# Performance work log

Hardware: AMD Instinct MI355X
Metric: run time of the kernel (lower is better)

The kernel has to match this reference:

```python
import jax, jax.numpy as jnp
import numpy as np

B, LQ, LK, H, A = 32, 2048, 2048, 1024, 512


def setup_inputs() -> dict:
    key = jax.random.key(0)
    ks = jax.random.split(key, 5)
    s = 1.0 / np.sqrt(H)
    return {
        "query": jax.random.normal(ks[0], (B, LQ, H), jnp.float32),
        "key": jax.random.normal(ks[1], (B, LK, H), jnp.float32),
        "Wq": jax.random.normal(ks[2], (H, A), jnp.float32) * s,
        "bq": jnp.zeros((A,), jnp.float32),
        "Wk": jax.random.normal(ks[3], (H, A), jnp.float32) * s,
        "bk": jnp.zeros((A,), jnp.float32),
        "Wv": jax.random.normal(ks[4], (A, 1), jnp.float32) * (1.0 / np.sqrt(A)),
        "bv": jnp.zeros((1,), jnp.float32),
    }


def reference(query, key, Wq, bq, Wk, bk, Wv, bv):
    # Linear projections
    Qp = jnp.einsum("bqh,ha->bqa", query, Wq) + bq          # [B, LQ, A]
    Kp = jnp.einsum("bkh,ha->bka", key, Wk) + bk            # [B, LK, A]
    # Score matrix Q(query) @ K(key)^T
    alpha_mat = jnp.einsum("bqa,bka->bqk", Qp, Kp)          # [B, LQ, LK]
    # Sum over query dim, softmax over key dim
    alpha = jax.nn.softmax(alpha_mat.sum(axis=1, keepdims=True), axis=2)  # [B, 1, LK]
    # Per-key scalar head V applied to projected keys, then weighted combine
    v = jnp.einsum("bka,ao->bko", Kp, Wv) + bv              # [B, LK, 1]
    x = jnp.matmul(alpha, v)[:, 0, :]                        # [B, 1]
    return x
```

## Files before the change

kernel.cpp:

```cpp
#include <hip/hip_runtime.h>
#include <math.h>

#define NB 32
#define LQ 2048
#define LK 2048
#define HD 1024
#define AD 512
#define QCH 32

__global__ void __launch_bounds__(256)
k1_stream(const float* __restrict__ query, const float* __restrict__ Wk,
          const float* __restrict__ Wv, const float* __restrict__ bk,
          const float* __restrict__ bv, float* __restrict__ partial,
          float* __restrict__ wv_eff, float* __restrict__ c_v) {
    const int bid = blockIdx.x;
    const int t = threadIdx.x;
    if (bid < NB * QCH) {
        int b = bid / QCH, qc = bid % QCH;
        const int QPC = LQ / QCH;
        float4 a0 = {0.f,0.f,0.f,0.f}, a1 = {0.f,0.f,0.f,0.f};
        float4 a2 = {0.f,0.f,0.f,0.f}, a3 = {0.f,0.f,0.f,0.f};
        const float4* src = (const float4*)(query + ((size_t)b * LQ + (size_t)qc * QPC) * HD);
        for (int q = 0; q < QPC; q += 4) {
            float4 v0 = src[(size_t)(q + 0) * (HD / 4) + t];
            float4 v1 = src[(size_t)(q + 1) * (HD / 4) + t];
            float4 v2 = src[(size_t)(q + 2) * (HD / 4) + t];
            float4 v3 = src[(size_t)(q + 3) * (HD / 4) + t];
            a0.x += v0.x; a0.y += v0.y; a0.z += v0.z; a0.w += v0.w;
            a1.x += v1.x; a1.y += v1.y; a1.z += v1.z; a1.w += v1.w;
            a2.x += v2.x; a2.y += v2.y; a2.z += v2.z; a2.w += v2.w;
            a3.x += v3.x; a3.y += v3.y; a3.z += v3.z; a3.w += v3.w;
        }
        float4 acc = {(a0.x + a1.x) + (a2.x + a3.x), (a0.y + a1.y) + (a2.y + a3.y),
                      (a0.z + a1.z) + (a2.z + a3.z), (a0.w + a1.w) + (a2.w + a3.w)};
        ((float4*)(partial + ((size_t)qc * NB + b) * HD))[t] = acc;
    } else if (bid < NB * QCH + 16) {
        int w = t >> 6, lane = t & 63;
        int gw = (bid - NB * QCH) * 4 + w;
        const float4* vv = (const float4*)Wv;
        for (int r = 0; r < 16; ++r) {
            int h = gw * 16 + r;
            const float4* wr = (const float4*)(Wk + (size_t)h * AD);
            double acc = 0.0;
            #pragma unroll
            for (int j = 0; j < 2; ++j) {
                int f = lane + 64 * j;
                float4 w4 = wr[f];
                float4 v4 = vv[f];
                acc += (double)w4.x * v4.x + (double)w4.y * v4.y
                     + (double)w4.z * v4.z + (double)w4.w * v4.w;
            }
            #pragma unroll
            for (int off = 32; off > 0; off >>= 1) acc += __shfl_down(acc, off);
            if (lane == 0) wv_eff[h] = (float)acc;
        }
    } else if (t < 64) {
        int lane = t;
        const float4* br = (const float4*)bk;
        const float4* vv = (const float4*)Wv;
        double acc = 0.0;
        #pragma unroll
        for (int j = 0; j < 2; ++j) {
            int f = lane + 64 * j;
            float4 b4 = br[f];
            float4 v4 = vv[f];
            acc += (double)b4.x * v4.x + (double)b4.y * v4.y
                 + (double)b4.z * v4.z + (double)b4.w * v4.w;
        }
        #pragma unroll
        for (int off = 32; off > 0; off >>= 1) acc += __shfl_down(acc, off);
        if (lane == 0) c_v[0] = (float)(acc + (double)bv[0]);
    }
}

__global__ void __launch_bounds__(256)
k2_qsum(const float* __restrict__ partial, const float* __restrict__ Wq,
        const float* __restrict__ bq, float* __restrict__ qsum) {
    __shared__ float sq[HD];
    __shared__ double red[4][64];
    int b = blockIdx.x >> 3;
    int a0 = (blockIdx.x & 7) * 64;
    int t = threadIdx.x;

    #pragma unroll
    for (int c = 0; c < 4; ++c) {
        int h = t + c * 256;
        float acc = 0.f;
        #pragma unroll 4
        for (int qc = 0; qc < QCH; ++qc)
            acc += partial[((size_t)qc * NB + b) * HD + h];
        sq[h] = acc;
    }
    __syncthreads();

    int w = t >> 6, lane = t & 63;
    int a = a0 + lane;
    const float* wp = Wq + a;
    double c0 = 0.0, c1 = 0.0, c2 = 0.0, c3 = 0.0;
    int hbase = w * 256;
    for (int i = 0; i < 256; i += 4) {
        int h = hbase + i;
        c0 += (double)sq[h]     * wp[(size_t)h * AD];
        c1 += (double)sq[h + 1] * wp[(size_t)(h + 1) * AD];
        c2 += (double)sq[h + 2] * wp[(size_t)(h + 2) * AD];
        c3 += (double)sq[h + 3] * wp[(size_t)(h + 3) * AD];
    }
    red[w][lane] = ((c0 + c1) + (c2 + c3));
    __syncthreads();
    if (t < 64) {
        double s = red[0][t] + red[1][t] + red[2][t] + red[3][t];
        qsum[(size_t)b * AD + a0 + t] = (float)(s + (double)LQ * bq[a0 + t]);
    }
}

__global__ void __launch_bounds__(256)
k3_weff(const float* __restrict__ qsum, const float* __restrict__ Wk,
        float* __restrict__ wk_eff) {
    int w = threadIdx.x >> 6, lane = threadIdx.x & 63;
    int widx = blockIdx.x * 4 + w;
    int base = widx * 4;
    for (int r = 0; r < 4; r += 2) {
        int idx0 = base + r;
        int b = idx0 >> 10, h0 = idx0 & (HD - 1);
        const float4* r0 = (const float4*)(Wk + (size_t)h0 * AD);
        const float4* r1 = (const float4*)(Wk + (size_t)(h0 + 1) * AD);
        const float4* qs = (const float4*)(qsum + (size_t)b * AD);
        double a0 = 0.0, a1 = 0.0;
        #pragma unroll
        for (int j = 0; j < 2; ++j) {
            int f = lane + 64 * j;
            float4 w0 = r0[f];
            float4 w1 = r1[f];
            float4 q4 = qs[f];
            a0 += (double)w0.x * q4.x + (double)w0.y * q4.y
                + (double)w0.z * q4.z + (double)w0.w * q4.w;
            a1 += (double)w1.x * q4.x + (double)w1.y * q4.y
                + (double)w1.z * q4.z + (double)w1.w * q4.w;
        }
        #pragma unroll
        for (int off = 32; off > 0; off >>= 1) {
            a0 += __shfl_down(a0, off);
            a1 += __shfl_down(a1, off);
        }
        if (lane == 0) {
            wk_eff[idx0]     = (float)a0;
            wk_eff[idx0 + 1] = (float)a1;
        }
    }
}

__global__ void __launch_bounds__(256)
k4_scores(const float* __restrict__ key, const float* __restrict__ wk_eff,
          const float* __restrict__ wv_eff, const float* __restrict__ c_v,
          float* __restrict__ scores, float* __restrict__ vvals) {
    __shared__ float lwk[HD];
    __shared__ float lwv[HD];
    const int bid = blockIdx.x;
    const int b = bid >> 6;
    const int k0 = (bid & 63) * 32;
    const int t = threadIdx.x;
    for (int i = t; i < HD; i += 256) {
        lwk[i] = wk_eff[(size_t)b * HD + i];
        lwv[i] = wv_eff[i];
    }
    __syncthreads();
    int w = t >> 6, lane = t & 63;
    double cv = (double)c_v[0];
    const float4* lwk4 = (const float4*)lwk;
    const float4* lwv4 = (const float4*)lwv;
    for (int rp = 0; rp < 2; ++rp) {
        int k = k0 + w * 8 + rp * 4;
        const float4* kr0 = (const float4*)(key + ((size_t)b * LK + k) * HD);
        const float4* kr1 = kr0 + (HD / 4);
        const float4* kr2 = kr0 + 2 * (HD / 4);
        const float4* kr3 = kr0 + 3 * (HD / 4);
        double sc0 = 0.0, vv0 = 0.0, sc1 = 0.0, vv1 = 0.0;
        double sc2 = 0.0, vv2 = 0.0, sc3 = 0.0, vv3 = 0.0;
        #pragma unroll
        for (int j = 0; j < 4; ++j) {
            int f = lane + 64 * j;
            float4 k0v = kr0[f];
            float4 k1v = kr1[f];
            float4 k2v = kr2[f];
            float4 k3v = kr3[f];
            float4 wk4 = lwk4[f];
            float4 wv4 = lwv4[f];
            sc0 += (double)k0v.x * wk4.x + (double)k0v.y * wk4.y
                 + (double)k0v.z * wk4.z + (double)k0v.w * wk4.w;
            vv0 += (double)k0v.x * wv4.x + (double)k0v.y * wv4.y
                 + (double)k0v.z * wv4.z + (double)k0v.w * wv4.w;
            sc1 += (double)k1v.x * wk4.x + (double)k1v.y * wk4.y
                 + (double)k1v.z * wk4.z + (double)k1v.w * wk4.w;
            vv1 += (double)k1v.x * wv4.x + (double)k1v.y * wv4.y
                 + (double)k1v.z * wv4.z + (double)k1v.w * wv4.w;
            sc2 += (double)k2v.x * wk4.x + (double)k2v.y * wk4.y
                 + (double)k2v.z * wk4.z + (double)k2v.w * wk4.w;
            vv2 += (double)k2v.x * wv4.x + (double)k2v.y * wv4.y
                 + (double)k2v.z * wv4.z + (double)k2v.w * wv4.w;
            sc3 += (double)k3v.x * wk4.x + (double)k3v.y * wk4.y
                 + (double)k3v.z * wk4.z + (double)k3v.w * wk4.w;
            vv3 += (double)k3v.x * wv4.x + (double)k3v.y * wv4.y
                 + (double)k3v.z * wv4.z + (double)k3v.w * wv4.w;
        }
        #pragma unroll
        for (int off = 32; off > 0; off >>= 1) {
            sc0 += __shfl_down(sc0, off);
            vv0 += __shfl_down(vv0, off);
            sc1 += __shfl_down(sc1, off);
            vv1 += __shfl_down(vv1, off);
            sc2 += __shfl_down(sc2, off);
            vv2 += __shfl_down(vv2, off);
            sc3 += __shfl_down(sc3, off);
            vv3 += __shfl_down(vv3, off);
        }
        if (lane == 0) {
            size_t base = (size_t)b * LK + k;
            scores[base]     = (float)sc0;  vvals[base]     = (float)(vv0 + cv);
            scores[base + 1] = (float)sc1;  vvals[base + 1] = (float)(vv1 + cv);
            scores[base + 2] = (float)sc2;  vvals[base + 2] = (float)(vv2 + cv);
            scores[base + 3] = (float)sc3;  vvals[base + 3] = (float)(vv3 + cv);
        }
    }
}

__global__ void __launch_bounds__(256)
k5_softmax(const float* __restrict__ scores, const float* __restrict__ vvals,
           float* __restrict__ out) {
    int b = blockIdx.x;
    int t = threadIdx.x;
    __shared__ float smax_sh[4];
    __shared__ double num_sh[4], den_sh[4];
    const float* sr = scores + (size_t)b * LK;
    const float* vr = vvals  + (size_t)b * LK;
    float m = -INFINITY;
    for (int k = t; k < LK; k += 256) m = fmaxf(m, sr[k]);
    #pragma unroll
    for (int off = 32; off > 0; off >>= 1) m = fmaxf(m, __shfl_down(m, off));
    int w = t >> 6, lane = t & 63;
    if (lane == 0) smax_sh[w] = m;
    __syncthreads();
    float gm = fmaxf(fmaxf(smax_sh[0], smax_sh[1]), fmaxf(smax_sh[2], smax_sh[3]));
    double num = 0.0, den = 0.0;
    for (int k = t; k < LK; k += 256) {
        double e = exp((double)(sr[k] - gm));
        den += e;
        num += e * (double)vr[k];
    }
    #pragma unroll
    for (int off = 32; off > 0; off >>= 1) {
        num += __shfl_down(num, off);
        den += __shfl_down(den, off);
    }
    if (lane == 0) { num_sh[w] = num; den_sh[w] = den; }
    __syncthreads();
    if (t == 0) {
        double N = num_sh[0] + num_sh[1] + num_sh[2] + num_sh[3];
        double D = den_sh[0] + den_sh[1] + den_sh[2] + den_sh[3];
        out[b] = (float)(N / D);
    }
}

extern "C" void kernel_launch(void* const* d_in, const int* in_sizes, int n_in,
                              void* d_out, int out_size, void* d_ws, size_t ws_size,
                              hipStream_t stream) {
    const float* query = (const float*)d_in[0];
    const float* key   = (const float*)d_in[1];
    const float* Wq    = (const float*)d_in[2];
    const float* bq    = (const float*)d_in[3];
    const float* Wk    = (const float*)d_in[4];
    const float* bk    = (const float*)d_in[5];
    const float* Wv    = (const float*)d_in[6];
    const float* bv    = (const float*)d_in[7];
    float* out = (float*)d_out;

    float* ws = (float*)d_ws;
    size_t off = 0;
    float* partial = ws + off; off += (size_t)QCH * NB * HD;
    float* qsum    = ws + off; off += (size_t)NB * AD;
    float* wk_eff  = ws + off; off += (size_t)NB * HD;
    float* wv_eff  = ws + off; off += (size_t)HD;
    float* c_v     = ws + off; off += 1;
    float* scores  = ws + off; off += (size_t)NB * LK;
    float* vvals   = ws + off; off += (size_t)NB * LK;

    hipLaunchKernelGGL(k1_stream, dim3(NB * QCH + 16 + 1), dim3(256), 0, stream,
                       query, Wk, Wv, bk, bv, partial, wv_eff, c_v);
    hipLaunchKernelGGL(k2_qsum, dim3(256), dim3(256), 0, stream,
                       partial, Wq, bq, qsum);
    hipLaunchKernelGGL(k3_weff, dim3(2048), dim3(256), 0, stream,
                       qsum, Wk, wk_eff);
    hipLaunchKernelGGL(k4_scores, dim3(NB * (LK / 32)), dim3(256), 0, stream,
                       key, wk_eff, wv_eff, c_v, scores, vvals);
    hipLaunchKernelGGL(k5_softmax, dim3(NB), dim3(256), 0, stream,
                       scores, vvals, out);
}
```

Measured before the change: 147.9 us.

## Fuse five kernels into two using last-block-done atomic counters

Merges the query-sum reduction, the Wq projection and the Wk effective-weight computation into the streaming kernel, and the softmax into the scores kernel. Each uses a per-batch atomic counter so that the last block to finish does the follow-up work. The streaming kernel now runs 512-thread blocks with float2 loads, and the counters are cleared with a memset. This removes three kernel launches and the intermediate round trips, but the fused tails (about 4 MB of weight reads per batch) now run on only 32 blocks instead of hundreds, which can lengthen the critical path.

```diff
diff --git a/kernel.cpp b/kernel.cpp
--- a/kernel.cpp
+++ b/kernel.cpp
@@ -8,38 +8,107 @@
 #define AD 512
 #define QCH 32
 
-__global__ void __launch_bounds__(256)
-k1_stream(const float* __restrict__ query, const float* __restrict__ Wk,
+__global__ void __launch_bounds__(512)
+k1_stream(const float* __restrict__ query, const float* __restrict__ Wq,
+          const float* __restrict__ bq, const float* __restrict__ Wk,
           const float* __restrict__ Wv, const float* __restrict__ bk,
-          const float* __restrict__ bv, float* __restrict__ partial,
-          float* __restrict__ wv_eff, float* __restrict__ c_v) {
+          const float* __restrict__ bv,
+          float* __restrict__ partial, float* __restrict__ wk_eff,
+          float* __restrict__ wv_eff, float* __restrict__ c_v,
+          int* __restrict__ cnt) {
+    __shared__ float sq[HD];
+    __shared__ float qs[AD];
+    __shared__ int isLast;
     const int bid = blockIdx.x;
     const int t = threadIdx.x;
+
     if (bid < NB * QCH) {
         int b = bid / QCH, qc = bid % QCH;
         const int QPC = LQ / QCH;
-        float4 a0 = {0.f,0.f,0.f,0.f}, a1 = {0.f,0.f,0.f,0.f};
-        float4 a2 = {0.f,0.f,0.f,0.f}, a3 = {0.f,0.f,0.f,0.f};
-        const float4* src = (const float4*)(query + ((size_t)b * LQ + (size_t)qc * QPC) * HD);
+        float2 a0 = {0.f,0.f}, a1 = {0.f,0.f}, a2 = {0.f,0.f}, a3 = {0.f,0.f};
+        const float2* src = (const float2*)(query + ((size_t)b * LQ + (size_t)qc * QPC) * HD);
         for (int q = 0; q < QPC; q += 4) {
-            float4 v0 = src[(size_t)(q + 0) * (HD / 4) + t];
-            float4 v1 = src[(size_t)(q + 1) * (HD / 4) + t];
-            float4 v2 = src[(size_t)(q + 2) * (HD / 4) + t];
-            float4 v3 = src[(size_t)(q + 3) * (HD / 4) + t];
-            a0.x += v0.x; a0.y += v0.y; a0.z += v0.z; a0.w += v0.w;
-            a1.x += v1.x; a1.y += v1.y; a1.z += v1.z; a1.w += v1.w;
-            a2.x += v2.x; a2.y += v2.y; a2.z += v2.z; a2.w += v2.w;
-            a3.x += v3.x; a3.y += v3.y; a3.z += v3.z; a3.w += v3.w;
-        }
-        float4 acc = {(a0.x + a1.x) + (a2.x + a3.x), (a0.y + a1.y) + (a2.y + a3.y),
-                      (a0.z + a1.z) + (a2.z + a3.z), (a0.w + a1.w) + (a2.w + a3.w)};
-        ((float4*)(partial + ((size_t)qc * NB + b) * HD))[t] = acc;
+            float2 v0 = src[(size_t)(q + 0) * (HD / 2) + t];
+            float2 v1 = src[(size_t)(q + 1) * (HD / 2) + t];
+            float2 v2 = src[(size_t)(q + 2) * (HD / 2) + t];
+            float2 v3 = src[(size_t)(q + 3) * (HD / 2) + t];
+            a0.x += v0.x; a0.y += v0.y;
+            a1.x += v1.x; a1.y += v1.y;
+            a2.x += v2.x; a2.y += v2.y;
+            a3.x += v3.x; a3.y += v3.y;
+        }
+        float sx = (a0.x + a1.x) + (a2.x + a3.x);
+        float sy = (a0.y + a1.y) + (a2.y + a3.y);
+        float* dst = partial + ((size_t)qc * NB + b) * HD + 2 * t;
+        atomicExch(dst,     sx);
+        atomicExch(dst + 1, sy);
+        asm volatile("s_waitcnt vmcnt(0)" ::: "memory");
+        __syncthreads();
+        if (t == 0) {
+            int old = atomicAdd(&cnt[b], 1);
+            isLast = (old == QCH - 1) ? 1 : 0;
+        }
+        __syncthreads();
+        if (!isLast) return;
+
+        #pragma unroll
+        for (int c = 0; c < 2; ++c) {
+            int h = t + c * 512;
+            float a = 0.f;
+            #pragma unroll 4
+            for (int q2 = 0; q2 < QCH; ++q2)
+                a += atomicAdd(partial + ((size_t)q2 * NB + b) * HD + h, 0.0f);
+            sq[h] = a;
+        }
+        __syncthreads();
+        {
+            const float* wp = Wq + t;
+            double c0 = 0.0, c1 = 0.0, c2 = 0.0, c3 = 0.0;
+            for (int h = 0; h < HD; h += 4) {
+                c0 += (double)sq[h]     * wp[(size_t)h * AD];
+                c1 += (double)sq[h + 1] * wp[(size_t)(h + 1) * AD];
+                c2 += (double)sq[h + 2] * wp[(size_t)(h + 2) * AD];
+                c3 += (double)sq[h + 3] * wp[(size_t)(h + 3) * AD];
+            }
+            qs[t] = (float)(((c0 + c1) + (c2 + c3)) + (double)LQ * (double)bq[t]);
+        }
+        __syncthreads();
+        {
+            int w = t >> 6, lane = t & 63;
+            const float4* qs4 = (const float4*)qs;
+            for (int r = 0; r < 128; r += 2) {
+                int h0 = w * 128 + r;
+                const float4* r0 = (const float4*)(Wk + (size_t)h0 * AD);
+                const float4* r1 = (const float4*)(Wk + (size_t)(h0 + 1) * AD);
+                double d0 = 0.0, d1 = 0.0;
+                #pragma unroll
+                for (int j = 0; j < 2; ++j) {
+                    int f = lane + 64 * j;
+                    float4 w0 = r0[f];
+                    float4 w1 = r1[f];
+                    float4 q4 = qs4[f];
+                    d0 += (double)w0.x * q4.x + (double)w0.y * q4.y
+                        + (double)w0.z * q4.z + (double)w0.w * q4.w;
+                    d1 += (double)w1.x * q4.x + (double)w1.y * q4.y
+                        + (double)w1.z * q4.z + (double)w1.w * q4.w;
+                }
+                #pragma unroll
+                for (int off = 32; off > 0; off >>= 1) {
+                    d0 += __shfl_down(d0, off);
+                    d1 += __shfl_down(d1, off);
+                }
+                if (lane == 0) {
+                    wk_eff[(size_t)b * HD + h0]     = (float)d0;
+                    wk_eff[(size_t)b * HD + h0 + 1] = (float)d1;
+                }
+            }
+        }
     } else if (bid < NB * QCH + 16) {
         int w = t >> 6, lane = t & 63;
-        int gw = (bid - NB * QCH) * 4 + w;
+        int gw = (bid - NB * QCH) * 8 + w;
         const float4* vv = (const float4*)Wv;
-        for (int r = 0; r < 16; ++r) {
-            int h = gw * 16 + r;
+        for (int r = 0; r < 8; ++r) {
+            int h = gw * 8 + r;
             const float4* wr = (const float4*)(Wk + (size_t)h * AD);
             double acc = 0.0;
             #pragma unroll
@@ -74,87 +143,15 @@
 }
 
 __global__ void __launch_bounds__(256)
-k2_qsum(const float* __restrict__ partial, const float* __restrict__ Wq,
-        const float* __restrict__ bq, float* __restrict__ qsum) {
-    __shared__ float sq[HD];
-    __shared__ double red[4][64];
-    int b = blockIdx.x >> 3;
-    int a0 = (blockIdx.x & 7) * 64;
-    int t = threadIdx.x;
-
-    #pragma unroll
-    for (int c = 0; c < 4; ++c) {
-        int h = t + c * 256;
-        float acc = 0.f;
-        #pragma unroll 4
-        for (int qc = 0; qc < QCH; ++qc)
-            acc += partial[((size_t)qc * NB + b) * HD + h];
-        sq[h] = acc;
-    }
-    __syncthreads();
-
-    int w = t >> 6, lane = t & 63;
-    int a = a0 + lane;
-    const float* wp = Wq + a;
-    double c0 = 0.0, c1 = 0.0, c2 = 0.0, c3 = 0.0;
-    int hbase = w * 256;
-    for (int i = 0; i < 256; i += 4) {
-        int h = hbase + i;
-        c0 += (double)sq[h]     * wp[(size_t)h * AD];
-        c1 += (double)sq[h + 1] * wp[(size_t)(h + 1) * AD];
-        c2 += (double)sq[h + 2] * wp[(size_t)(h + 2) * AD];
-        c3 += (double)sq[h + 3] * wp[(size_t)(h + 3) * AD];
-    }
-    red[w][lane] = ((c0 + c1) + (c2 + c3));
-    __syncthreads();
-    if (t < 64) {
-        double s = red[0][t] + red[1][t] + red[2][t] + red[3][t];
-        qsum[(size_t)b * AD + a0 + t] = (float)(s + (double)LQ * bq[a0 + t]);
-    }
-}
-
-__global__ void __launch_bounds__(256)
-k3_weff(const float* __restrict__ qsum, const float* __restrict__ Wk,
-        float* __restrict__ wk_eff) {
-    int w = threadIdx.x >> 6, lane = threadIdx.x & 63;
-    int widx = blockIdx.x * 4 + w;
-    int base = widx * 4;
-    for (int r = 0; r < 4; r += 2) {
-        int idx0 = base + r;
-        int b = idx0 >> 10, h0 = idx0 & (HD - 1);
-        const float4* r0 = (const float4*)(Wk + (size_t)h0 * AD);
-        const float4* r1 = (const float4*)(Wk + (size_t)(h0 + 1) * AD);
-        const float4* qs = (const float4*)(qsum + (size_t)b * AD);
-        double a0 = 0.0, a1 = 0.0;
-        #pragma unroll
-        for (int j = 0; j < 2; ++j) {
-            int f = lane + 64 * j;
-            float4 w0 = r0[f];
-            float4 w1 = r1[f];
-            float4 q4 = qs[f];
-            a0 += (double)w0.x * q4.x + (double)w0.y * q4.y
-                + (double)w0.z * q4.z + (double)w0.w * q4.w;
-            a1 += (double)w1.x * q4.x + (double)w1.y * q4.y
-                + (double)w1.z * q4.z + (double)w1.w * q4.w;
-        }
-        #pragma unroll
-        for (int off = 32; off > 0; off >>= 1) {
-            a0 += __shfl_down(a0, off);
-            a1 += __shfl_down(a1, off);
-        }
-        if (lane == 0) {
-            wk_eff[idx0]     = (float)a0;
-            wk_eff[idx0 + 1] = (float)a1;
-        }
-    }
-}
-
-__global__ void __launch_bounds__(256)
-k4_scores(const float* __restrict__ key, const float* __restrict__ wk_eff,
+k2_scores(const float* __restrict__ key, const float* __restrict__ wk_eff,
           const float* __restrict__ wv_eff, const float* __restrict__ c_v,
-          float* __restrict__ scores, float* __restrict__ vvals) {
+          float* __restrict__ scores, float* __restrict__ vvals,
+          int* __restrict__ cnt2, float* __restrict__ out) {
     __shared__ float lwk[HD];
     __shared__ float lwv[HD];
+    __shared__ int isLast;
+    __shared__ float smax_sh[4];
+    __shared__ double num_sh[4], den_sh[4];
     const int bid = blockIdx.x;
     const int b = bid >> 6;
     const int k0 = (bid & 63) * 32;
@@ -215,36 +212,46 @@
         }
         if (lane == 0) {
             size_t base = (size_t)b * LK + k;
-            scores[base]     = (float)sc0;  vvals[base]     = (float)(vv0 + cv);
-            scores[base + 1] = (float)sc1;  vvals[base + 1] = (float)(vv1 + cv);
-            scores[base + 2] = (float)sc2;  vvals[base + 2] = (float)(vv2 + cv);
-            scores[base + 3] = (float)sc3;  vvals[base + 3] = (float)(vv3 + cv);
-        }
-    }
-}
-
-__global__ void __launch_bounds__(256)
-k5_softmax(const float* __restrict__ scores, const float* __restrict__ vvals,
-           float* __restrict__ out) {
-    int b = blockIdx.x;
-    int t = threadIdx.x;
-    __shared__ float smax_sh[4];
-    __shared__ double num_sh[4], den_sh[4];
-    const float* sr = scores + (size_t)b * LK;
-    const float* vr = vvals  + (size_t)b * LK;
-    float m = -INFINITY;
-    for (int k = t; k < LK; k += 256) m = fmaxf(m, sr[k]);
+            atomicExch(&scores[base],     (float)sc0);
+            atomicExch(&vvals [base],     (float)(vv0 + cv));
+            atomicExch(&scores[base + 1], (float)sc1);
+            atomicExch(&vvals [base + 1], (float)(vv1 + cv));
+            atomicExch(&scores[base + 2], (float)sc2);
+            atomicExch(&vvals [base + 2], (float)(vv2 + cv));
+            atomicExch(&scores[base + 3], (float)sc3);
+            atomicExch(&vvals [base + 3], (float)(vv3 + cv));
+        }
+    }
+    asm volatile("s_waitcnt vmcnt(0)" ::: "memory");
+    __syncthreads();
+    if (t == 0) {
+        int old = atomicAdd(&cnt2[b], 1);
+        isLast = (old == 63) ? 1 : 0;
+    }
+    __syncthreads();
+    if (!isLast) return;
+
+    float s8[8], v8[8];
+    #pragma unroll
+    for (int i = 0; i < 8; ++i) {
+        int k = t + i * 256;
+        s8[i] = atomicAdd(&scores[(size_t)b * LK + k], 0.0f);
+        v8[i] = atomicAdd(&vvals [(size_t)b * LK + k], 0.0f);
+    }
+    float m = s8[0];
+    #pragma unroll
+    for (int i = 1; i < 8; ++i) m = fmaxf(m, s8[i]);
     #pragma unroll
     for (int off = 32; off > 0; off >>= 1) m = fmaxf(m, __shfl_down(m, off));
-    int w = t >> 6, lane = t & 63;
     if (lane == 0) smax_sh[w] = m;
     __syncthreads();
     float gm = fmaxf(fmaxf(smax_sh[0], smax_sh[1]), fmaxf(smax_sh[2], smax_sh[3]));
     double num = 0.0, den = 0.0;
-    for (int k = t; k < LK; k += 256) {
-        double e = exp((double)(sr[k] - gm));
+    #pragma unroll
+    for (int i = 0; i < 8; ++i) {
+        double e = exp((double)s8[i] - (double)gm);
         den += e;
-        num += e * (double)vr[k];
+        num += e * (double)v8[i];
     }
     #pragma unroll
     for (int off = 32; off > 0; off >>= 1) {
@@ -276,21 +283,17 @@
     float* ws = (float*)d_ws;
     size_t off = 0;
     float* partial = ws + off; off += (size_t)QCH * NB * HD;
-    float* qsum    = ws + off; off += (size_t)NB * AD;
     float* wk_eff  = ws + off; off += (size_t)NB * HD;
     float* wv_eff  = ws + off; off += (size_t)HD;
     float* c_v     = ws + off; off += 1;
     float* scores  = ws + off; off += (size_t)NB * LK;
     float* vvals   = ws + off; off += (size_t)NB * LK;
-
-    hipLaunchKernelGGL(k1_stream, dim3(NB * QCH + 16 + 1), dim3(256), 0, stream,
-                       query, Wk, Wv, bk, bv, partial, wv_eff, c_v);
-    hipLaunchKernelGGL(k2_qsum, dim3(256), dim3(256), 0, stream,
-                       partial, Wq, bq, qsum);
-    hipLaunchKernelGGL(k3_weff, dim3(2048), dim3(256), 0, stream,
-                       qsum, Wk, wk_eff);
-    hipLaunchKernelGGL(k4_scores, dim3(NB * (LK / 32)), dim3(256), 0, stream,
-                       key, wk_eff, wv_eff, c_v, scores, vvals);
-    hipLaunchKernelGGL(k5_softmax, dim3(NB), dim3(256), 0, stream,
-                       scores, vvals, out);
+    int*   cnt     = (int*)(ws + off); off += 2 * NB;
+
+    hipMemsetAsync(cnt, 0, 2 * NB * sizeof(int), stream);
+    hipLaunchKernelGGL(k1_stream, dim3(NB * QCH + 16 + 1), dim3(512), 0, stream,
+                       query, Wq, bq, Wk, Wv, bk, bv,
+                       partial, wk_eff, wv_eff, c_v, cnt);
+    hipLaunchKernelGGL(k2_scores, dim3(NB * (LK / 32)), dim3(256), 0, stream,
+                       key, wk_eff, wv_eff, c_v, scores, vvals, cnt + NB, out);
 }
```

After: 277.5 us. 87.5% more time.

## Fuse softmax-weighted combine into scores kernel via last-block reduction

Applied to the files above, without the earlier changes.

Drops the separate softmax kernel. Each scores block now computes a local max, exp-sum and weighted sum over its 32 keys and publishes them to a workspace with atomics. The last block per batch, found through an atomic counter, merges the 64 partials with max rescaling and writes the output. This removes one kernel launch and the global round trip of the scores and values, at the cost of an extra memset, atomic traffic and a serialized tail block per batch.

```diff
diff --git a/kernel.cpp b/kernel.cpp
--- a/kernel.cpp
+++ b/kernel.cpp
@@ -152,12 +152,17 @@
 __global__ void __launch_bounds__(256)
 k4_scores(const float* __restrict__ key, const float* __restrict__ wk_eff,
           const float* __restrict__ wv_eff, const float* __restrict__ c_v,
-          float* __restrict__ scores, float* __restrict__ vvals) {
+          double* __restrict__ pub, int* __restrict__ cnt,
+          float* __restrict__ out) {
     __shared__ float lwk[HD];
     __shared__ float lwv[HD];
+    __shared__ double sLDS[32];
+    __shared__ double vLDS[32];
+    __shared__ int isLast;
     const int bid = blockIdx.x;
     const int b = bid >> 6;
-    const int k0 = (bid & 63) * 32;
+    const int j = bid & 63;
+    const int k0 = j * 32;
     const int t = threadIdx.x;
     for (int i = t; i < HD; i += 256) {
         lwk[i] = wk_eff[(size_t)b * HD + i];
@@ -177,8 +182,8 @@
         double sc0 = 0.0, vv0 = 0.0, sc1 = 0.0, vv1 = 0.0;
         double sc2 = 0.0, vv2 = 0.0, sc3 = 0.0, vv3 = 0.0;
         #pragma unroll
-        for (int j = 0; j < 4; ++j) {
-            int f = lane + 64 * j;
+        for (int jj = 0; jj < 4; ++jj) {
+            int f = lane + 64 * jj;
             float4 k0v = kr0[f];
             float4 k1v = kr1[f];
             float4 k2v = kr2[f];
@@ -214,49 +219,61 @@
             vv3 += __shfl_down(vv3, off);
         }
         if (lane == 0) {
-            size_t base = (size_t)b * LK + k;
-            scores[base]     = (float)sc0;  vvals[base]     = (float)(vv0 + cv);
-            scores[base + 1] = (float)sc1;  vvals[base + 1] = (float)(vv1 + cv);
-            scores[base + 2] = (float)sc2;  vvals[base + 2] = (float)(vv2 + cv);
-            scores[base + 3] = (float)sc3;  vvals[base + 3] = (float)(vv3 + cv);
-        }
-    }
-}
-
-__global__ void __launch_bounds__(256)
-k5_softmax(const float* __restrict__ scores, const float* __restrict__ vvals,
-           float* __restrict__ out) {
-    int b = blockIdx.x;
-    int t = threadIdx.x;
-    __shared__ float smax_sh[4];
-    __shared__ double num_sh[4], den_sh[4];
-    const float* sr = scores + (size_t)b * LK;
-    const float* vr = vvals  + (size_t)b * LK;
-    float m = -INFINITY;
-    for (int k = t; k < LK; k += 256) m = fmaxf(m, sr[k]);
-    #pragma unroll
-    for (int off = 32; off > 0; off >>= 1) m = fmaxf(m, __shfl_down(m, off));
-    int w = t >> 6, lane = t & 63;
-    if (lane == 0) smax_sh[w] = m;
-    __syncthreads();
-    float gm = fmaxf(fmaxf(smax_sh[0], smax_sh[1]), fmaxf(smax_sh[2], smax_sh[3]));
-    double num = 0.0, den = 0.0;
-    for (int k = t; k < LK; k += 256) {
-        double e = exp((double)(sr[k] - gm));
-        den += e;
-        num += e * (double)vr[k];
-    }
-    #pragma unroll
-    for (int off = 32; off > 0; off >>= 1) {
-        num += __shfl_down(num, off);
-        den += __shfl_down(den, off);
-    }
-    if (lane == 0) { num_sh[w] = num; den_sh[w] = den; }
-    __syncthreads();
-    if (t == 0) {
-        double N = num_sh[0] + num_sh[1] + num_sh[2] + num_sh[3];
-        double D = den_sh[0] + den_sh[1] + den_sh[2] + den_sh[3];
-        out[b] = (float)(N / D);
+            int kl = w * 8 + rp * 4;
+            sLDS[kl]     = sc0;  vLDS[kl]     = vv0 + cv;
+            sLDS[kl + 1] = sc1;  vLDS[kl + 1] = vv1 + cv;
+            sLDS[kl + 2] = sc2;  vLDS[kl + 2] = vv2 + cv;
+            sLDS[kl + 3] = sc3;  vLDS[kl + 3] = vv3 + cv;
+        }
+    }
+    __syncthreads();
+
+    if (w == 0) {
+        double s = sLDS[lane & 31];
+        double m = s;
+        #pragma unroll
+        for (int off = 32; off > 0; off >>= 1) m = fmax(m, __shfl_down(m, off));
+        m = __shfl(m, 0);
+        double e = (lane < 32) ? exp(s - m) : 0.0;
+        double ev = (lane < 32) ? e * vLDS[lane] : 0.0;
+        #pragma unroll
+        for (int off = 32; off > 0; off >>= 1) {
+            e  += __shfl_down(e, off);
+            ev += __shfl_down(ev, off);
+        }
+        if (lane == 0) {
+            unsigned long long* p =
+                (unsigned long long*)(pub + ((size_t)b * 64 + j) * 3);
+            atomicExch(&p[0], __double_as_longlong(m));
+            atomicExch(&p[1], __double_as_longlong(e));
+            atomicExch(&p[2], __double_as_longlong(ev));
+            asm volatile("s_waitcnt vmcnt(0)" ::: "memory");
+            int old = atomicAdd(&cnt[b], 1);
+            isLast = (old == 63) ? 1 : 0;
+        }
+    }
+    __syncthreads();
+    if (!isLast) return;
+
+    if (w == 0) {
+        unsigned long long* pb =
+            (unsigned long long*)(pub + (size_t)b * 64 * 3);
+        double mj = __longlong_as_double(atomicAdd(&pb[lane * 3 + 0], 0ull));
+        double Dj = __longlong_as_double(atomicAdd(&pb[lane * 3 + 1], 0ull));
+        double Nj = __longlong_as_double(atomicAdd(&pb[lane * 3 + 2], 0ull));
+        double m = mj;
+        #pragma unroll
+        for (int off = 32; off > 0; off >>= 1) m = fmax(m, __shfl_down(m, off));
+        m = __shfl(m, 0);
+        double sc = exp(mj - m);
+        double D = Dj * sc;
+        double N = Nj * sc;
+        #pragma unroll
+        for (int off = 32; off > 0; off >>= 1) {
+            D += __shfl_down(D, off);
+            N += __shfl_down(N, off);
+        }
+        if (lane == 0) out[b] = (float)(N / D);
     }
 }
 
@@ -279,10 +296,11 @@
     float* qsum    = ws + off; off += (size_t)NB * AD;
     float* wk_eff  = ws + off; off += (size_t)NB * HD;
     float* wv_eff  = ws + off; off += (size_t)HD;
-    float* c_v     = ws + off; off += 1;
-    float* scores  = ws + off; off += (size_t)NB * LK;
-    float* vvals   = ws + off; off += (size_t)NB * LK;
-
+    float* c_v     = ws + off; off += 2;
+    double* pub    = (double*)(ws + off); off += (size_t)NB * 64 * 3 * 2;
+    int*   cnt     = (int*)(ws + off); off += NB;
+
+    hipMemsetAsync(cnt, 0, NB * sizeof(int), stream);
     hipLaunchKernelGGL(k1_stream, dim3(NB * QCH + 16 + 1), dim3(256), 0, stream,
                        query, Wk, Wv, bk, bv, partial, wv_eff, c_v);
     hipLaunchKernelGGL(k2_qsum, dim3(256), dim3(256), 0, stream,
@@ -290,7 +308,5 @@
     hipLaunchKernelGGL(k3_weff, dim3(2048), dim3(256), 0, stream,
                        qsum, Wk, wk_eff);
     hipLaunchKernelGGL(k4_scores, dim3(NB * (LK / 32)), dim3(256), 0, stream,
-                       key, wk_eff, wv_eff, c_v, scores, vvals);
-    hipLaunchKernelGGL(k5_softmax, dim3(NB), dim3(256), 0, stream,
-                       scores, vvals, out);
-}
+                       key, wk_eff, wv_eff, c_v, pub, cnt, out);
+}
```

After: 155.6 us. 5.2% more time.

## Precompute Wk·Wq^T during query streaming and fold two reduction kernels into one

Applied to the files above, without the earlier changes.

Reassociates the query-sum path. Instead of computing qsum = sum(query)·Wq and then Wk·qsum per batch in two kernels, the first kernel now also builds the 1024x1024 matrix M = Wk·Wq^T with a shared-memory tiled fp32 GEMM. Those GEMM blocks run alongside the query-streaming blocks, along with the bias term ck = LQ·Wk·bq. A single follow-up kernel then computes wk_eff = M·sum(query) + ck. This removes one dependent launch and the serialized qsum stage, at the cost of an extra 0.5 GFLOP GEMM, a 4 MB intermediate, and fp32 rather than double accumulation for the M products.

```diff
diff --git a/kernel.cpp b/kernel.cpp
--- a/kernel.cpp
+++ b/kernel.cpp
@@ -8,15 +8,21 @@
 #define AD 512
 #define QCH 32
 
-__global__ void __launch_bounds__(256)
-k1_stream(const float* __restrict__ query, const float* __restrict__ Wk,
-          const float* __restrict__ Wv, const float* __restrict__ bk,
-          const float* __restrict__ bv, float* __restrict__ partial,
-          float* __restrict__ wv_eff, float* __restrict__ c_v) {
+__global__ void __launch_bounds__(256, 4)
+k1_main(const float* __restrict__ query, const float* __restrict__ Wq,
+        const float* __restrict__ Wk, const float* __restrict__ Wv,
+        const float* __restrict__ bq, const float* __restrict__ bk,
+        const float* __restrict__ bv, float* __restrict__ partial,
+        float* __restrict__ MT, float* __restrict__ wv_eff,
+        float* __restrict__ ck, float* __restrict__ c_v) {
+    __shared__ float wq_l[128][33];
+    __shared__ float wk_l[32][33];
     const int bid = blockIdx.x;
     const int t = threadIdx.x;
-    if (bid < NB * QCH) {
-        int b = bid / QCH, qc = bid % QCH;
+
+    if (bid >= 256) {
+        int task = bid - 256;
+        int b = task / QCH, qc = task % QCH;
         const int QPC = LQ / QCH;
         float4 a0 = {0.f,0.f,0.f,0.f}, a1 = {0.f,0.f,0.f,0.f};
         float4 a2 = {0.f,0.f,0.f,0.f}, a3 = {0.f,0.f,0.f,0.f};
@@ -34,57 +40,100 @@
         float4 acc = {(a0.x + a1.x) + (a2.x + a3.x), (a0.y + a1.y) + (a2.y + a3.y),
                       (a0.z + a1.z) + (a2.z + a3.z), (a0.w + a1.w) + (a2.w + a3.w)};
         ((float4*)(partial + ((size_t)qc * NB + b) * HD))[t] = acc;
-    } else if (bid < NB * QCH + 16) {
+        return;
+    }
+
+    const int hb = bid >> 3;
+    const int pb = bid & 7;
+    const int hgrp = t >> 5;
+    const int pgrp = t & 31;
+    float acc[4][4] = {{0.f}};
+    for (int ac = 0; ac < 16; ++ac) {
+        for (int s = t; s < 128 * 32; s += 256) {
+            int row = s >> 5, a = s & 31;
+            wq_l[row][a] = Wq[(size_t)(pb * 128 + row) * AD + ac * 32 + a];
+        }
+        for (int s = t; s < 32 * 32; s += 256) {
+            int row = s >> 5, a = s & 31;
+            wk_l[row][a] = Wk[(size_t)(hb * 32 + row) * AD + ac * 32 + a];
+        }
+        __syncthreads();
+        #pragma unroll 8
+        for (int a = 0; a < 32; ++a) {
+            float k0 = wk_l[hgrp][a],      k1 = wk_l[hgrp + 8][a],
+                  k2 = wk_l[hgrp + 16][a], k3 = wk_l[hgrp + 24][a];
+            float q0 = wq_l[pgrp][a],      q1 = wq_l[pgrp + 32][a],
+                  q2 = wq_l[pgrp + 64][a], q3 = wq_l[pgrp + 96][a];
+            acc[0][0] += k0*q0; acc[0][1] += k0*q1; acc[0][2] += k0*q2; acc[0][3] += k0*q3;
+            acc[1][0] += k1*q0; acc[1][1] += k1*q1; acc[1][2] += k1*q2; acc[1][3] += k1*q3;
+            acc[2][0] += k2*q0; acc[2][1] += k2*q1; acc[2][2] += k2*q2; acc[2][3] += k2*q3;
+            acc[3][0] += k3*q0; acc[3][1] += k3*q1; acc[3][2] += k3*q2; acc[3][3] += k3*q3;
+        }
+        __syncthreads();
+    }
+    #pragma unroll
+    for (int i = 0; i < 4; ++i)
+        #pragma unroll
+        for (int j = 0; j < 4; ++j)
+            MT[(size_t)(hb * 32 + hgrp + 8 * i) * HD + pb * 128 + pgrp + 32 * j] = acc[i][j];
+
+    if (pb == 0) {
         int w = t >> 6, lane = t & 63;
-        int gw = (bid - NB * QCH) * 4 + w;
-        const float4* vv = (const float4*)Wv;
-        for (int r = 0; r < 16; ++r) {
-            int h = gw * 16 + r;
+        const float4* vv4 = (const float4*)Wv;
+        const float4* bq4 = (const float4*)bq;
+        for (int rr = 0; rr < 8; ++rr) {
+            int h = hb * 32 + w * 8 + rr;
             const float4* wr = (const float4*)(Wk + (size_t)h * AD);
-            double acc = 0.0;
+            double a1 = 0.0, a2 = 0.0;
             #pragma unroll
             for (int j = 0; j < 2; ++j) {
                 int f = lane + 64 * j;
                 float4 w4 = wr[f];
-                float4 v4 = vv[f];
-                acc += (double)w4.x * v4.x + (double)w4.y * v4.y
-                     + (double)w4.z * v4.z + (double)w4.w * v4.w;
+                float4 v4 = vv4[f];
+                float4 b4 = bq4[f];
+                a1 += (double)w4.x * v4.x + (double)w4.y * v4.y
+                    + (double)w4.z * v4.z + (double)w4.w * v4.w;
+                a2 += (double)b4.x * w4.x + (double)b4.y * w4.y
+                    + (double)b4.z * w4.z + (double)b4.w * w4.w;
             }
             #pragma unroll
-            for (int off = 32; off > 0; off >>= 1) acc += __shfl_down(acc, off);
-            if (lane == 0) wv_eff[h] = (float)acc;
-        }
-    } else if (t < 64) {
+            for (int off = 32; off > 0; off >>= 1) {
+                a1 += __shfl_down(a1, off);
+                a2 += __shfl_down(a2, off);
+            }
+            if (lane == 0) {
+                wv_eff[h] = (float)a1;
+                ck[h] = (float)((double)LQ * a2);
+            }
+        }
+    }
+    if (bid == 0 && t < 64) {
         int lane = t;
         const float4* br = (const float4*)bk;
-        const float4* vv = (const float4*)Wv;
-        double acc = 0.0;
+        const float4* vv4 = (const float4*)Wv;
+        double acc2 = 0.0;
         #pragma unroll
         for (int j = 0; j < 2; ++j) {
             int f = lane + 64 * j;
             float4 b4 = br[f];
-            float4 v4 = vv[f];
-            acc += (double)b4.x * v4.x + (double)b4.y * v4.y
-                 + (double)b4.z * v4.z + (double)b4.w * v4.w;
-        }
-        #pragma unroll
-        for (int off = 32; off > 0; off >>= 1) acc += __shfl_down(acc, off);
-        if (lane == 0) c_v[0] = (float)(acc + (double)bv[0]);
+            float4 v4 = vv4[f];
+            acc2 += (double)b4.x * v4.x + (double)b4.y * v4.y
+                  + (double)b4.z * v4.z + (double)b4.w * v4.w;
+        }
+        #pragma unroll
+        for (int off = 32; off > 0; off >>= 1) acc2 += __shfl_down(acc2, off);
+        if (lane == 0) c_v[0] = (float)(acc2 + (double)bv[0]);
     }
 }
 
 __global__ void __launch_bounds__(256)
-k2_qsum(const float* __restrict__ partial, const float* __restrict__ Wq,
-        const float* __restrict__ bq, float* __restrict__ qsum) {
+k2_wkeff(const float* __restrict__ partial, const float* __restrict__ MT,
+         const float* __restrict__ ck, float* __restrict__ wk_eff) {
     __shared__ float sq[HD];
-    __shared__ double red[4][64];
-    int b = blockIdx.x >> 3;
-    int a0 = (blockIdx.x & 7) * 64;
-    int t = threadIdx.x;
-
-    #pragma unroll
-    for (int c = 0; c < 4; ++c) {
-        int h = t + c * 256;
+    const int bid = blockIdx.x;
+    const int t = threadIdx.x;
+    const int b = bid >> 3, hc = bid & 7;
+    for (int h = t; h < HD; h += 256) {
         float acc = 0.f;
         #pragma unroll 4
         for (int qc = 0; qc < QCH; ++qc)
@@ -92,60 +141,23 @@
         sq[h] = acc;
     }
     __syncthreads();
-
     int w = t >> 6, lane = t & 63;
-    int a = a0 + lane;
-    const float* wp = Wq + a;
-    double c0 = 0.0, c1 = 0.0, c2 = 0.0, c3 = 0.0;
-    int hbase = w * 256;
-    for (int i = 0; i < 256; i += 4) {
-        int h = hbase + i;
-        c0 += (double)sq[h]     * wp[(size_t)h * AD];
-        c1 += (double)sq[h + 1] * wp[(size_t)(h + 1) * AD];
-        c2 += (double)sq[h + 2] * wp[(size_t)(h + 2) * AD];
-        c3 += (double)sq[h + 3] * wp[(size_t)(h + 3) * AD];
-    }
-    red[w][lane] = ((c0 + c1) + (c2 + c3));
-    __syncthreads();
-    if (t < 64) {
-        double s = red[0][t] + red[1][t] + red[2][t] + red[3][t];
-        qsum[(size_t)b * AD + a0 + t] = (float)(s + (double)LQ * bq[a0 + t]);
-    }
-}
-
-__global__ void __launch_bounds__(256)
-k3_weff(const float* __restrict__ qsum, const float* __restrict__ Wk,
-        float* __restrict__ wk_eff) {
-    int w = threadIdx.x >> 6, lane = threadIdx.x & 63;
-    int widx = blockIdx.x * 4 + w;
-    int base = widx * 4;
-    for (int r = 0; r < 4; r += 2) {
-        int idx0 = base + r;
-        int b = idx0 >> 10, h0 = idx0 & (HD - 1);
-        const float4* r0 = (const float4*)(Wk + (size_t)h0 * AD);
-        const float4* r1 = (const float4*)(Wk + (size_t)(h0 + 1) * AD);
-        const float4* qs = (const float4*)(qsum + (size_t)b * AD);
-        double a0 = 0.0, a1 = 0.0;
-        #pragma unroll
-        for (int j = 0; j < 2; ++j) {
-            int f = lane + 64 * j;
-            float4 w0 = r0[f];
-            float4 w1 = r1[f];
-            float4 q4 = qs[f];
-            a0 += (double)w0.x * q4.x + (double)w0.y * q4.y
-                + (double)w0.z * q4.z + (double)w0.w * q4.w;
-            a1 += (double)w1.x * q4.x + (double)w1.y * q4.y
-                + (double)w1.z * q4.z + (double)w1.w * q4.w;
-        }
-        #pragma unroll
-        for (int off = 32; off > 0; off >>= 1) {
-            a0 += __shfl_down(a0, off);
-            a1 += __shfl_down(a1, off);
-        }
-        if (lane == 0) {
-            wk_eff[idx0]     = (float)a0;
-            wk_eff[idx0 + 1] = (float)a1;
-        }
+    const float4* sq4 = (const float4*)sq;
+    for (int rr = 0; rr < 32; ++rr) {
+        int h = hc * 128 + w * 32 + rr;
+        const float4* m4 = (const float4*)(MT + (size_t)h * HD);
+        double acc = 0.0;
+        #pragma unroll
+        for (int f0 = 0; f0 < 4; ++f0) {
+            int f = lane + 64 * f0;
+            float4 m = m4[f];
+            float4 s = sq4[f];
+            acc += (double)m.x * s.x + (double)m.y * s.y
+                 + (double)m.z * s.z + (double)m.w * s.w;
+        }
+        #pragma unroll
+        for (int off = 32; off > 0; off >>= 1) acc += __shfl_down(acc, off);
+        if (lane == 0) wk_eff[(size_t)b * HD + h] = (float)(acc + (double)ck[h]);
     }
 }
 
@@ -276,19 +288,19 @@
     float* ws = (float*)d_ws;
     size_t off = 0;
     float* partial = ws + off; off += (size_t)QCH * NB * HD;
-    float* qsum    = ws + off; off += (size_t)NB * AD;
+    float* MT      = ws + off; off += (size_t)HD * HD;
     float* wk_eff  = ws + off; off += (size_t)NB * HD;
     float* wv_eff  = ws + off; off += (size_t)HD;
+    float* ck      = ws + off; off += (size_t)HD;
     float* c_v     = ws + off; off += 1;
     float* scores  = ws + off; off += (size_t)NB * LK;
     float* vvals   = ws + off; off += (size_t)NB * LK;
 
-    hipLaunchKernelGGL(k1_stream, dim3(NB * QCH + 16 + 1), dim3(256), 0, stream,
-                       query, Wk, Wv, bk, bv, partial, wv_eff, c_v);
-    hipLaunchKernelGGL(k2_qsum, dim3(256), dim3(256), 0, stream,
-                       partial, Wq, bq, qsum);
-    hipLaunchKernelGGL(k3_weff, dim3(2048), dim3(256), 0, stream,
-                       qsum, Wk, wk_eff);
+    hipLaunchKernelGGL(k1_main, dim3(256 + NB * QCH), dim3(256), 0, stream,
+                       query, Wq, Wk, Wv, bq, bk, bv,
+                       partial, MT, wv_eff, ck, c_v);
+    hipLaunchKernelGGL(k2_wkeff, dim3(256), dim3(256), 0, stream,
+                       partial, MT, ck, wk_eff);
     hipLaunchKernelGGL(k4_scores, dim3(NB * (LK / 32)), dim3(256), 0, stream,
                        key, wk_eff, wv_eff, c_v, scores, vvals);
     hipLaunchKernelGGL(k5_softmax, dim3(NB), dim3(256), 0, stream,
```

Result: slower. 201.7 us (+36.4%).
